# Optimization experiments

Hardware: AMD Instinct MI355X
Metric: run time of the kernel (lower is better)

Reference implementation:

```python
import jax, jax.numpy as jnp
import numpy as np

WS = 4        # window_size
HEADS = 12    # num_heads


def setup_inputs() -> dict:
    key = jax.random.key(0)
    k1, k2, k3 = jax.random.split(key, 3)
    B, N, E = 32, 4096, 384
    x = jax.random.normal(k1, (B, N, E), dtype=jnp.float32)
    w_in = jax.random.normal(k2, (3 * E, E), dtype=jnp.float32) * 0.02
    b_in = jnp.zeros((3 * E,), dtype=jnp.float32)
    w_out = jax.random.normal(k3, (E, E), dtype=jnp.float32) * 0.02
    b_out = jnp.zeros((E,), dtype=jnp.float32)
    return {"x": x, "w_in": w_in, "b_in": b_in, "w_out": w_out, "b_out": b_out}


def reference(x, w_in, b_in, w_out, b_out):
    B, N, E = x.shape
    H = W = int(np.sqrt(N))
    nh, nw = H // WS, W // WS
    hd = E // HEADS
    T = WS * WS  # tokens per window

    # window partition: [B, H, W, E] -> [B*nh*nw, T, E]
    xw = x.reshape(B, nh, WS, nw, WS, E)
    xw = xw.transpose(0, 1, 3, 2, 4, 5).reshape(-1, T, E)

    # packed QKV projection (torch nn.MultiheadAttention in_proj)
    qkv = xw @ w_in.T + b_in                      # [nWin, T, 3E]
    q, k, v = jnp.split(qkv, 3, axis=-1)          # each [nWin, T, E]

    def split_heads(t):
        return t.reshape(-1, T, HEADS, hd).transpose(0, 2, 1, 3)  # [nWin, h, T, hd]

    q, k, v = split_heads(q), split_heads(k), split_heads(v)
    scale = 1.0 / np.sqrt(hd).astype(np.float32)
    scores = jnp.einsum('whqd,whkd->whqk', q * scale, k)          # [nWin, h, T, T]
    attn = jax.nn.softmax(scores, axis=-1)
    out = jnp.einsum('whqk,whkd->whqd', attn, v)                  # [nWin, h, T, hd]
    out = out.transpose(0, 2, 1, 3).reshape(-1, T, E)
    out = out @ w_out.T + b_out                                   # out_proj

    # window reverse: [B*nh*nw, T, E] -> [B, N, E]
    out = out.reshape(B, nh, nw, WS, WS, E)
    out = out.transpose(0, 1, 3, 2, 4, 5).reshape(B, N, E)
    return out
```

## Files before the change

kernel.cpp:

```cpp
#include <hip/hip_runtime.h>
#include <hip/hip_bf16.h>

typedef __attribute__((ext_vector_type(8))) short short8;
typedef __attribute__((ext_vector_type(4))) float f32x4;

static __device__ __forceinline__ f32x4 MFMA16(short8 a, short8 b, f32x4 c) {
    return __builtin_amdgcn_mfma_f32_16x16x32_bf16(a, b, c, 0, 0, 0);
}
static __device__ __forceinline__ unsigned short f2bf(float f) {
    union { __hip_bfloat16 h; unsigned short u; } c;
    c.h = __float2bfloat16(f);
    return c.u;
}
static __device__ __forceinline__ void gload16(const void* g, void* l) {
    __builtin_amdgcn_global_load_lds(
        (const __attribute__((address_space(1))) unsigned int*)g,
        (__attribute__((address_space(3))) unsigned int*)l, 16, 0, 0);
}

constexpr size_t kWstOff = 0;
constexpr size_t kWosOff = 884736;
constexpr size_t kBrrOff = 1179648;
constexpr size_t kAttOff = 1184256;

__global__ void prep(const float* __restrict__ w_in, const float* __restrict__ b_in,
                     const float* __restrict__ w_out,
                     char* __restrict__ wst, char* __restrict__ wos,
                     float* __restrict__ brr)
{
    const int i = blockIdx.x * 256 + threadIdx.x;
    if (i < 55296) {
        int hp = i / 9216, rem = i % 9216;
        int s = rem / 1536, slot16 = rem % 1536;
        int row = slot16 >> 3, sl = slot16 & 7;
        int c8 = sl ^ (row & 7);
        int hh = row / 96, rr = row % 96;
        int sec = rr >> 5, d = rr & 31;
        int srow = sec * 384 + (hp * 2 + hh) * 32 + d;
        int k0 = s * 64 + c8 * 8;
        const float4* src = (const float4*)(w_in + (size_t)srow * 384 + k0);
        float4 a = src[0], b = src[1];
        uint4 w;
        w.x = f2bf(a.x) | ((unsigned)f2bf(a.y) << 16);
        w.y = f2bf(a.z) | ((unsigned)f2bf(a.w) << 16);
        w.z = f2bf(b.x) | ((unsigned)f2bf(b.y) << 16);
        w.w = f2bf(b.z) | ((unsigned)f2bf(b.w) << 16);
        *(uint4*)(wst + (size_t)i * 16) = w;
    } else {
        int j = i - 55296;
        int nb = j / 6144, rem = j % 6144;
        int s = rem / 1024, slot16 = rem % 1024;
        int row = slot16 >> 3, sl = slot16 & 7;
        int c8 = sl ^ (row & 7);
        int srow = nb * 128 + row;
        int k0 = s * 64 + c8 * 8;
        const float4* src = (const float4*)(w_out + (size_t)srow * 384 + k0);
        float4 a = src[0], b = src[1];
        uint4 w;
        w.x = f2bf(a.x) | ((unsigned)f2bf(a.y) << 16);
        w.y = f2bf(a.z) | ((unsigned)f2bf(a.w) << 16);
        w.z = f2bf(b.x) | ((unsigned)f2bf(b.y) << 16);
        w.w = f2bf(b.z) | ((unsigned)f2bf(b.w) << 16);
        *(uint4*)(wos + (size_t)j * 16) = w;
    }
    if (i < 1152) {
        int h = i / 96, jj = i % 96;
        int sec = jj >> 5, d = jj & 31;
        brr[i] = b_in[sec * 384 + h * 32 + d];
    }
}

__global__ __launch_bounds__(512, 4)
void qkv_attn(const float* __restrict__ x, const char* __restrict__ wst,
              const float* __restrict__ brr, char* __restrict__ attst)
{
    __shared__ __align__(16) char smem[49152];

    const int tid  = threadIdx.x;
    const int lane = tid & 63, wid = tid >> 6;
    const int g = lane >> 4, r16 = lane & 15;
    const int wm = wid >> 1, wn = wid & 1;

    int b = blockIdx.x;
    int L = (b & 7) * 768 + (b >> 3);
    const int mblk = L / 6, hp = L - mblk * 6;
    const int head = hp * 2 + wn;

    const int arow = tid >> 2, aq = tid & 3;
    int T0 = mblk * 128 + arow;
    int win0 = T0 >> 4, t4 = T0 & 15;
    int bb0 = win0 >> 8, wh = (win0 >> 4) & 15, ww = win0 & 15;
    const float* xrow = x + ((size_t)bb0 * 4096 +
                             (size_t)((wh * 4 + (t4 >> 2)) * 64 + ww * 4 + (t4 & 3))) * 384
                          + aq * 16;

    float4 af[4];
    auto load_A = [&](int s) {
        const float4* xp = (const float4*)(xrow + s * 64);
        #pragma unroll
        for (int j = 0; j < 4; ++j) af[j] = xp[j];
    };
    auto write_A = [&]() {
        #pragma unroll
        for (int j = 0; j < 2; ++j) {
            uint4 w;
            w.x = f2bf(af[2*j].x)   | ((unsigned)f2bf(af[2*j].y)   << 16);
            w.y = f2bf(af[2*j].z)   | ((unsigned)f2bf(af[2*j].w)   << 16);
            w.z = f2bf(af[2*j+1].x) | ((unsigned)f2bf(af[2*j+1].y) << 16);
            w.w = f2bf(af[2*j+1].z) | ((unsigned)f2bf(af[2*j+1].w) << 16);
            int slot = (aq * 2 + j) ^ (arow & 7);
            *(uint4*)(smem + arow * 128 + slot * 16) = w;
        }
    };
    const char* wst_blk = wst + (size_t)hp * 147456;
    auto stage_B = [&](int s) {
        char* dst = smem + 16384 + tid * 16;
        const char* src = wst_blk + s * 24576 + tid * 16;
        #pragma unroll
        for (int j = 0; j < 3; ++j) gload16(src + j * 8192, dst + j * 8192);
    };

    f32x4 acc[2][6] = {};
    auto compute = [&]() {
        #pragma unroll
        for (int c = 0; c < 2; ++c) {
            const int sw = ((c * 4 + g) ^ (r16 & 7)) << 4;
            short8 a[2], bf[6];
            #pragma unroll
            for (int mi = 0; mi < 2; ++mi)
                a[mi] = *(const short8*)(smem + (wm * 32 + mi * 16 + r16) * 128 + sw);
            #pragma unroll
            for (int ni = 0; ni < 6; ++ni)
                bf[ni] = *(const short8*)(smem + 16384 + (wn * 96 + ni * 16 + r16) * 128 + sw);
            #pragma unroll
            for (int mi = 0; mi < 2; ++mi)
                #pragma unroll
                for (int ni = 0; ni < 6; ++ni)
                    acc[mi][ni] = MFMA16(a[mi], bf[ni], acc[mi][ni]);
        }
    };

    load_A(0);
    stage_B(0);
    write_A();
    for (int s = 0; s < 6; ++s) {
        __syncthreads();
        if (s < 5) load_A(s + 1);
        compute();
        if (s < 5) {
            __syncthreads();
            stage_B(s + 1);
            write_A();
        }
    }
    __syncthreads();

    float bias[6];
    #pragma unroll
    for (int ni = 0; ni < 6; ++ni) bias[ni] = brr[head * 96 + ni * 16 + r16];

    #pragma unroll
    for (int mi = 0; mi < 2; ++mi) {
        const int win = wm * 2 + mi;
        #pragma unroll
        for (int ni = 0; ni < 6; ++ni) {
            const int sec = ni >> 1;
            const int d = (ni & 1) * 16 + r16;
            float v0 = acc[mi][ni][0] + bias[ni];
            float v1 = acc[mi][ni][1] + bias[ni];
            float v2 = acc[mi][ni][2] + bias[ni];
            float v3 = acc[mi][ni][3] + bias[ni];
            uint2 w;
            w.x = f2bf(v0) | ((unsigned)f2bf(v1) << 16);
            w.y = f2bf(v2) | ((unsigned)f2bf(v3) << 16);
            *(uint2*)(smem + win * 6144 + wn * 3072 + sec * 1024 + d * 32 + g * 8) = w;
        }
    }

    const float kC = 0.17677669529663687f * 1.4426950408889634f;
    const f32x4 zero = {0.f, 0.f, 0.f, 0.f};

    #pragma unroll
    for (int i = 0; i < 2; ++i) {
        const int win = wm * 2 + i;
        const char* base = smem + win * 6144 + wn * 3072;

        union U8 { unsigned short e[8]; short8 v; };
        U8 ku, qu;
        #pragma unroll
        for (int j = 0; j < 8; ++j) {
            const int off = (g * 8 + j) * 32 + r16 * 2;
            qu.e[j] = *(const unsigned short*)(base + off);
            ku.e[j] = *(const unsigned short*)(base + 1024 + off);
        }
        f32x4 s = MFMA16(ku.v, qu.v, zero);

        float m = fmaxf(fmaxf(s[0], s[1]), fmaxf(s[2], s[3]));
        m = fmaxf(m, __shfl_xor(m, 16, 64));
        m = fmaxf(m, __shfl_xor(m, 32, 64));
        float p[4], sum = 0.f;
        #pragma unroll
        for (int r = 0; r < 4; ++r) { p[r] = exp2f((s[r] - m) * kC); sum += p[r]; }
        sum += __shfl_xor(sum, 16, 64);
        sum += __shfl_xor(sum, 32, 64);
        const float inv = 1.f / sum;

        U8 pu;
        pu.e[0] = f2bf(p[0] * inv); pu.e[1] = f2bf(p[1] * inv);
        pu.e[2] = f2bf(p[2] * inv); pu.e[3] = f2bf(p[3] * inv);
        pu.e[4] = 0; pu.e[5] = 0; pu.e[6] = 0; pu.e[7] = 0;

        f32x4 o[2];
        #pragma unroll
        for (int ti = 0; ti < 2; ++ti) {
            U8 vu;
            *(uint2*)&vu.e[0] = *(const uint2*)(base + 2048 + (ti * 16 + r16) * 32 + g * 8);
            vu.e[4] = 0; vu.e[5] = 0; vu.e[6] = 0; vu.e[7] = 0;
            o[ti] = MFMA16(pu.v, vu.v, zero);
        }
        #pragma unroll
        for (int ti = 0; ti < 2; ++ti) {
            #pragma unroll
            for (int r = 0; r < 4; ++r) {
                int row7 = win * 16 + g * 4 + r;
                int col = head * 32 + ti * 16 + r16;
                int sst = col >> 6;
                int sl = ((col >> 3) & 7) ^ (row7 & 7);
                *(unsigned short*)(attst + (size_t)mblk * 98304 + sst * 16384
                                   + row7 * 128 + sl * 16 + (col & 7) * 2)
                    = f2bf(o[ti][r]);
            }
        }
    }
}

__global__ __launch_bounds__(256, 2)
void out_proj(const char* __restrict__ attst, const char* __restrict__ wos,
              const float* __restrict__ b_out, float* __restrict__ out)
{
    __shared__ __align__(16) char smem[65536];

    const int tid  = threadIdx.x;
    const int lane = tid & 63, wid = tid >> 6;
    const int g = lane >> 4, r16 = lane & 15;
    const int wm = wid >> 1, wn = wid & 1;

    int b = blockIdx.x;
    int L = (b & 7) * 384 + (b >> 3);
    const int mblk = L / 3, nblk = L - mblk * 3;

    auto stage = [&](int s, int buf) {
        const char* asrc = attst + (size_t)mblk * 98304 + s * 16384 + wid * 4096 + lane * 16;
        const char* bsrc = wos   + (size_t)nblk * 98304 + s * 16384 + wid * 4096 + lane * 16;
        char* adst = smem + buf * 16384 + wid * 4096;
        char* bdst = smem + 32768 + buf * 16384 + wid * 4096;
        #pragma unroll
        for (int j = 0; j < 4; ++j) {
            gload16(asrc + j * 1024, adst + j * 1024);
            gload16(bsrc + j * 1024, bdst + j * 1024);
        }
    };

    f32x4 acc[4][4] = {};
    auto compute = [&](int buf) {
        const char* ab = smem + buf * 16384;
        const char* bbp = smem + 32768 + buf * 16384;
        #pragma unroll
        for (int c = 0; c < 2; ++c) {
            const int sw = ((c * 4 + g) ^ (r16 & 7)) << 4;
            short8 a[4], bf[4];
            #pragma unroll
            for (int mi = 0; mi < 4; ++mi)
                a[mi] = *(const short8*)(ab + (wm * 64 + mi * 16 + r16) * 128 + sw);
            #pragma unroll
            for (int ni = 0; ni < 4; ++ni)
                bf[ni] = *(const short8*)(bbp + (wn * 64 + ni * 16 + r16) * 128 + sw);
            #pragma unroll
            for (int mi = 0; mi < 4; ++mi)
                #pragma unroll
                for (int ni = 0; ni < 4; ++ni)
                    acc[mi][ni] = MFMA16(a[mi], bf[ni], acc[mi][ni]);
        }
    };

    stage(0, 0);
    for (int s = 0; s < 6; ++s) {
        __syncthreads();
        if (s < 5) stage(s + 1, (s + 1) & 1);
        compute(s & 1);
    }

    float bias[4];
    #pragma unroll
    for (int ni = 0; ni < 4; ++ni) bias[ni] = b_out[nblk * 128 + wn * 64 + ni * 16 + r16];

    #pragma unroll
    for (int mi = 0; mi < 4; ++mi) {
        #pragma unroll
        for (int r = 0; r < 4; ++r) {
            int T = mblk * 128 + wm * 64 + mi * 16 + g * 4 + r;
            int win = T >> 4, tt = T & 15;
            int bb = win >> 8, wh = (win >> 4) & 15, ww = win & 15;
            size_t o = ((size_t)bb * 4096 + (wh * 4 + (tt >> 2)) * 64 + ww * 4 + (tt & 3)) * 384
                     + nblk * 128 + wn * 64;
            #pragma unroll
            for (int ni = 0; ni < 4; ++ni)
                out[o + ni * 16 + r16] = acc[mi][ni][r] + bias[ni];
        }
    }
}

extern "C" void kernel_launch(void* const* d_in, const int* in_sizes, int n_in,
                              void* d_out, int out_size, void* d_ws, size_t ws_size,
                              hipStream_t stream) {
    const float* x     = (const float*)d_in[0];
    const float* w_in  = (const float*)d_in[1];
    const float* b_in  = (const float*)d_in[2];
    const float* w_out = (const float*)d_in[3];
    const float* b_out = (const float*)d_in[4];
    float* out = (float*)d_out;

    char* ws = (char*)d_ws;
    char*  wst = ws + kWstOff;
    char*  wos = ws + kWosOff;
    float* brr = (float*)(ws + kBrrOff);
    char*  att = ws + kAttOff;

    prep<<<dim3(288), dim3(256), 0, stream>>>(w_in, b_in, w_out, wst, wos, brr);
    qkv_attn<<<dim3(6144), dim3(512), 0, stream>>>(x, wst, brr, att);
    out_proj<<<dim3(3072), dim3(256), 0, stream>>>(att, wos, b_out, out);
}
```

Before: 283.2 us.

## Halve qkv_attn M-tile to 64 rows for smaller LDS and higher occupancy

The QKV+attention kernel now processes 64 tokens (4 windows) per block instead of 128, and the 8 waves are re-split as 2x4 over the 64x192 output tile. LDS use drops from 48KB to 32KB and launch bounds rise to 6 blocks/SM, with twice as many blocks. The aim is more occupancy and latency hiding. The cost is that the B-weight tile is reloaded twice as often per token. An extra barrier is added before attention because each wave now computes one window-head pair from data written by other waves.

Result: slower. 296.0 us (+4.5%).

```diff
diff --git a/kernel.cpp b/kernel.cpp
--- a/kernel.cpp
+++ b/kernel.cpp
@@ -70,72 +70,67 @@
     }
 }
 
-__global__ __launch_bounds__(512, 4)
+__global__ __launch_bounds__(512, 6)
 void qkv_attn(const float* __restrict__ x, const char* __restrict__ wst,
               const float* __restrict__ brr, char* __restrict__ attst)
 {
-    __shared__ __align__(16) char smem[49152];
+    __shared__ __align__(16) char smem[32768];
 
     const int tid  = threadIdx.x;
     const int lane = tid & 63, wid = tid >> 6;
     const int g = lane >> 4, r16 = lane & 15;
-    const int wm = wid >> 1, wn = wid & 1;
+    const int wm = wid >> 2, wn = wid & 3;
 
     int b = blockIdx.x;
-    int L = (b & 7) * 768 + (b >> 3);
+    int L = (b & 7) * 1536 + (b >> 3);
     const int mblk = L / 6, hp = L - mblk * 6;
-    const int head = hp * 2 + wn;
-
-    const int arow = tid >> 2, aq = tid & 3;
-    int T0 = mblk * 128 + arow;
+
+    const int arow = tid >> 3, aq = tid & 7;
+    int T0 = mblk * 64 + arow;
     int win0 = T0 >> 4, t4 = T0 & 15;
     int bb0 = win0 >> 8, wh = (win0 >> 4) & 15, ww = win0 & 15;
     const float* xrow = x + ((size_t)bb0 * 4096 +
                              (size_t)((wh * 4 + (t4 >> 2)) * 64 + ww * 4 + (t4 & 3))) * 384
-                          + aq * 16;
-
-    float4 af[4];
+                          + aq * 8;
+
+    float4 af[2];
     auto load_A = [&](int s) {
         const float4* xp = (const float4*)(xrow + s * 64);
-        #pragma unroll
-        for (int j = 0; j < 4; ++j) af[j] = xp[j];
+        af[0] = xp[0]; af[1] = xp[1];
     };
     auto write_A = [&]() {
-        #pragma unroll
-        for (int j = 0; j < 2; ++j) {
-            uint4 w;
-            w.x = f2bf(af[2*j].x)   | ((unsigned)f2bf(af[2*j].y)   << 16);
-            w.y = f2bf(af[2*j].z)   | ((unsigned)f2bf(af[2*j].w)   << 16);
-            w.z = f2bf(af[2*j+1].x) | ((unsigned)f2bf(af[2*j+1].y) << 16);
-            w.w = f2bf(af[2*j+1].z) | ((unsigned)f2bf(af[2*j+1].w) << 16);
-            int slot = (aq * 2 + j) ^ (arow & 7);
-            *(uint4*)(smem + arow * 128 + slot * 16) = w;
-        }
+        uint4 w;
+        w.x = f2bf(af[0].x) | ((unsigned)f2bf(af[0].y) << 16);
+        w.y = f2bf(af[0].z) | ((unsigned)f2bf(af[0].w) << 16);
+        w.z = f2bf(af[1].x) | ((unsigned)f2bf(af[1].y) << 16);
+        w.w = f2bf(af[1].z) | ((unsigned)f2bf(af[1].w) << 16);
+        int slot = aq ^ (arow & 7);
+        *(uint4*)(smem + arow * 128 + slot * 16) = w;
     };
     const char* wst_blk = wst + (size_t)hp * 147456;
     auto stage_B = [&](int s) {
-        char* dst = smem + 16384 + tid * 16;
+        char* dst = smem + 8192 + tid * 16;
         const char* src = wst_blk + s * 24576 + tid * 16;
         #pragma unroll
         for (int j = 0; j < 3; ++j) gload16(src + j * 8192, dst + j * 8192);
     };
 
-    f32x4 acc[2][6] = {};
+    f32x4 acc[2][3] = {};
     auto compute = [&]() {
         #pragma unroll
         for (int c = 0; c < 2; ++c) {
             const int sw = ((c * 4 + g) ^ (r16 & 7)) << 4;
-            short8 a[2], bf[6];
+            short8 a[2], bf[3];
             #pragma unroll
             for (int mi = 0; mi < 2; ++mi)
                 a[mi] = *(const short8*)(smem + (wm * 32 + mi * 16 + r16) * 128 + sw);
             #pragma unroll
-            for (int ni = 0; ni < 6; ++ni)
-                bf[ni] = *(const short8*)(smem + 16384 + (wn * 96 + ni * 16 + r16) * 128 + sw);
+            for (int ni = 0; ni < 3; ++ni)
+                bf[ni] = *(const short8*)(smem + 8192 + (wn * 48 + ni * 16 + r16) * 128 + sw);
             #pragma unroll
             for (int mi = 0; mi < 2; ++mi)
                 #pragma unroll
-                for (int ni = 0; ni < 6; ++ni)
+                for (int ni = 0; ni < 3; ++ni)
                     acc[mi][ni] = MFMA16(a[mi], bf[ni], acc[mi][ni]);
         }
     };
@@ -155,35 +150,35 @@
     }
     __syncthreads();
 
-    float bias[6];
-    #pragma unroll
-    for (int ni = 0; ni < 6; ++ni) bias[ni] = brr[head * 96 + ni * 16 + r16];
-
     #pragma unroll
     for (int mi = 0; mi < 2; ++mi) {
         const int win = wm * 2 + mi;
         #pragma unroll
-        for (int ni = 0; ni < 6; ++ni) {
-            const int sec = ni >> 1;
-            const int d = (ni & 1) * 16 + r16;
-            float v0 = acc[mi][ni][0] + bias[ni];
-            float v1 = acc[mi][ni][1] + bias[ni];
-            float v2 = acc[mi][ni][2] + bias[ni];
-            float v3 = acc[mi][ni][3] + bias[ni];
+        for (int ni = 0; ni < 3; ++ni) {
+            const int cb = wn * 48 + ni * 16;
+            const int hl = cb / 96;
+            const int w96 = cb - hl * 96;
+            const int sec = w96 >> 5;
+            const int d = (w96 & 31) + r16;
+            const float bias = brr[(hp * 2 + hl) * 96 + w96 + r16];
+            float v0 = acc[mi][ni][0] + bias;
+            float v1 = acc[mi][ni][1] + bias;
+            float v2 = acc[mi][ni][2] + bias;
+            float v3 = acc[mi][ni][3] + bias;
             uint2 w;
             w.x = f2bf(v0) | ((unsigned)f2bf(v1) << 16);
             w.y = f2bf(v2) | ((unsigned)f2bf(v3) << 16);
-            *(uint2*)(smem + win * 6144 + wn * 3072 + sec * 1024 + d * 32 + g * 8) = w;
-        }
-    }
+            *(uint2*)(smem + win * 6144 + hl * 3072 + sec * 1024 + d * 32 + g * 8) = w;
+        }
+    }
+    __syncthreads();
 
     const float kC = 0.17677669529663687f * 1.4426950408889634f;
     const f32x4 zero = {0.f, 0.f, 0.f, 0.f};
-
-    #pragma unroll
-    for (int i = 0; i < 2; ++i) {
-        const int win = wm * 2 + i;
-        const char* base = smem + win * 6144 + wn * 3072;
+    {
+        const int win = wid >> 1;
+        const int hl  = wid & 1;
+        const char* base = smem + win * 6144 + hl * 3072;
 
         union U8 { unsigned short e[8]; short8 v; };
         U8 ku, qu;
@@ -218,15 +213,17 @@
             vu.e[4] = 0; vu.e[5] = 0; vu.e[6] = 0; vu.e[7] = 0;
             o[ti] = MFMA16(pu.v, vu.v, zero);
         }
+        const int ghead = hp * 2 + hl;
         #pragma unroll
         for (int ti = 0; ti < 2; ++ti) {
             #pragma unroll
             for (int r = 0; r < 4; ++r) {
-                int row7 = win * 16 + g * 4 + r;
-                int col = head * 32 + ti * 16 + r16;
+                int gr = mblk * 64 + win * 16 + g * 4 + r;
+                int mb = gr >> 7, row7 = gr & 127;
+                int col = ghead * 32 + ti * 16 + r16;
                 int sst = col >> 6;
                 int sl = ((col >> 3) & 7) ^ (row7 & 7);
-                *(unsigned short*)(attst + (size_t)mblk * 98304 + sst * 16384
+                *(unsigned short*)(attst + (size_t)mb * 98304 + sst * 16384
                                    + row7 * 128 + sl * 16 + (col & 7) * 2)
                     = f2bf(o[ti][r]);
             }
@@ -327,6 +324,6 @@
     char*  att = ws + kAttOff;
 
     prep<<<dim3(288), dim3(256), 0, stream>>>(w_in, b_in, w_out, wst, wos, brr);
-    qkv_attn<<<dim3(6144), dim3(512), 0, stream>>>(x, wst, brr, att);
+    qkv_attn<<<dim3(12288), dim3(512), 0, stream>>>(x, wst, brr, att);
     out_proj<<<dim3(3072), dim3(256), 0, stream>>>(att, wos, b_out, out);
 }
```
